# Kernel optimization log

Measured on AMD Instinct MI355X. Metric: run time of the kernel, lower is better.

## Reference

```python
import jax, jax.numpy as jnp
import numpy as np

N_RAYS = 65536
COUNT_CYCLE = (32, 64, 128, 256)  # ragged per-ray sample counts, avg 120
N_TOTAL = N_RAYS // len(COUNT_CYCLE) * sum(COUNT_CYCLE)  # 7,864,320


def _build_rays_a():
    counts = np.tile(np.array(COUNT_CYCLE, dtype=np.int32), N_RAYS // len(COUNT_CYCLE))
    starts = np.concatenate([[0], np.cumsum(counts)[:-1]]).astype(np.int32)
    ray_idx = np.arange(N_RAYS, dtype=np.int32)
    return jnp.asarray(np.stack([ray_idx, starts, counts], axis=1))


def setup_inputs() -> dict:
    key = jax.random.key(0)
    k1, k2, k3, k4 = jax.random.split(key, 4)
    sigmas = jax.random.uniform(k1, (N_TOTAL,), dtype=jnp.float32) * 2.0   # nonneg densities
    rgbs = jax.random.uniform(k2, (N_TOTAL, 3), dtype=jnp.float32)
    deltas = jax.random.uniform(k3, (N_TOTAL,), dtype=jnp.float32) * 0.05  # step sizes
    ts = jnp.sort(jax.random.uniform(k4, (N_TOTAL,), dtype=jnp.float32)) * 4.0
    rays_a = _build_rays_a()
    T_threshold = jnp.array([1e-4], dtype=jnp.float32)
    return {"sigmas": sigmas, "rgbs": rgbs, "deltas": deltas, "ts": ts,
            "rays_a": rays_a, "T_threshold": T_threshold}


def reference(sigmas, rgbs, deltas, ts, rays_a, T_threshold):
    """Per-ray alpha compositing with early termination (T >= thr).

    Within a ray, transmittance T is the exclusive product of (1 - a) with
    a = 1 - exp(-sigma*delta), i.e. T = exp(-cumsum_excl(sigma*delta)).
    Since T is monotone non-increasing, the kernel's sequential early-exit
    (skip samples once T < thr) equals masking with the prefix T >= thr.
    """
    n_rays = rays_a.shape[0]
    n = sigmas.shape[0]
    starts = rays_a[:, 1]
    # ray id of every flat sample (segments are contiguous, sorted starts)
    rid = jnp.searchsorted(starts, jnp.arange(n, dtype=starts.dtype), side="right") - 1

    sd = sigmas * deltas                      # [N]
    cs = jnp.cumsum(sd)
    excl = cs - sd                            # exclusive cumsum over the flat buffer
    seg_base = jnp.where(starts > 0, cs[jnp.maximum(starts - 1, 0)], 0.0)  # [n_rays]
    T = jnp.exp(-(excl - seg_base[rid]))      # exclusive transmittance within ray

    a = 1.0 - jnp.exp(-sd)
    alive = T >= T_threshold[0]               # prefix mask == early exit
    w = jnp.where(alive, a * T, 0.0)          # per-sample weights (ws)

    opacity = jax.ops.segment_sum(w, rid, num_segments=n_rays)
    depth = jax.ops.segment_sum(w * ts, rid, num_segments=n_rays)
    rgb = jax.ops.segment_sum(w[:, None] * rgbs, rid, num_segments=n_rays)
    total_samples = jax.ops.segment_sum(alive.astype(jnp.int32), rid, num_segments=n_rays)
    return total_samples, opacity, depth, rgb, w
```

## Files before the change

kernel.cpp:

```cpp
#include <hip/hip_runtime.h>


__global__ __launch_bounds__(256) void vr_fwd_kernel(
    const float* __restrict__ sigmas,
    const float* __restrict__ rgbs,
    const float* __restrict__ deltas,
    const float* __restrict__ ts,
    const int*   __restrict__ rays_a,
    const float* __restrict__ thr_p,
    float* __restrict__ out,
    int n_rays)
{
    const int wid  = (int)((blockIdx.x * (unsigned)blockDim.x + threadIdx.x) >> 6);
    const int lane = (int)(threadIdx.x & 63u);
    if (wid >= n_rays) return;

    const int   start = rays_a[wid * 3 + 1];
    const int   count = rays_a[wid * 3 + 2];
    const float thr   = thr_p[0];

    float* __restrict__ out_counts  = out;
    float* __restrict__ out_opacity = out + n_rays;
    float* __restrict__ out_depth   = out + 2 * n_rays;
    float* __restrict__ out_rgb     = out + 3 * n_rays;
    float* __restrict__ out_w       = out + 6 * n_rays;

    float carry = 0.0f;
    float acc_n = 0.0f, acc_op = 0.0f, acc_d = 0.0f;
    float acc_r = 0.0f, acc_g = 0.0f, acc_b = 0.0f;

    for (int base = 0; base < count; base += 64) {
        const int  i     = base + lane;
        const bool valid = (i < count);
        const int  gi    = start + i;

        float sd = 0.0f;
        if (valid) sd = sigmas[gi] * deltas[gi];

        float scan = sd;
        #pragma unroll
        for (int off = 1; off < 64; off <<= 1) {
            float up = __shfl_up(scan, off, 64);
            if (lane >= off) scan += up;
        }
        const float total = __shfl(scan, 63, 64);
        const float excl  = carry + (scan - sd);
        carry += total;

        if (valid) {
            const float T     = __expf(-excl);
            const float a     = 1.0f - __expf(-sd);
            const bool  alive = (T >= thr);
            const float w     = alive ? a * T : 0.0f;
            out_w[gi] = w;
            if (alive) {
                acc_n  += 1.0f;
                acc_op += w;
                acc_d  += w * ts[gi];
                acc_r  += w * rgbs[gi * 3 + 0];
                acc_g  += w * rgbs[gi * 3 + 1];
                acc_b  += w * rgbs[gi * 3 + 2];
            }
        }
    }

    #pragma unroll
    for (int off = 32; off > 0; off >>= 1) {
        acc_n  += __shfl_down(acc_n,  off, 64);
        acc_op += __shfl_down(acc_op, off, 64);
        acc_d  += __shfl_down(acc_d,  off, 64);
        acc_r  += __shfl_down(acc_r,  off, 64);
        acc_g  += __shfl_down(acc_g,  off, 64);
        acc_b  += __shfl_down(acc_b,  off, 64);
    }

    if (lane == 0) {
        out_counts[wid]      = acc_n;
        out_opacity[wid]     = acc_op;
        out_depth[wid]       = acc_d;
        out_rgb[wid * 3 + 0] = acc_r;
        out_rgb[wid * 3 + 1] = acc_g;
        out_rgb[wid * 3 + 2] = acc_b;
    }
}

extern "C" void kernel_launch(void* const* d_in, const int* in_sizes, int n_in,
                              void* d_out, int out_size, void* d_ws, size_t ws_size,
                              hipStream_t stream) {
    const float* sigmas = (const float*)d_in[0];
    const float* rgbs   = (const float*)d_in[1];
    const float* deltas = (const float*)d_in[2];
    const float* ts     = (const float*)d_in[3];
    const int*   rays_a = (const int*)d_in[4];
    const float* thr    = (const float*)d_in[5];

    const int n_rays = in_sizes[4] / 3;
    float* out = (float*)d_out;

    const int blocks = (n_rays + 3) / 4;
    vr_fwd_kernel<<<blocks, 256, 0, stream>>>(sigmas, rgbs, deltas, ts, rays_a,
                                              thr, out, n_rays);
}
```

Baseline: 44.94 us.

## Process four samples per lane with vectorized float4 loads and stores

Each lane now handles four consecutive samples, loading sigmas, deltas, ts and the interleaved rgb values as float4 when the ray start is 4-aligned, and writing weights as float4. A local 4-element prefix sum feeds a single wave scan per 256 samples, and transmittance within a lane is updated by multiplying by exp(-sd) instead of a separate exp per sample. This cuts shuffle-scan steps and memory instructions per sample. In exchange it adds a scalar fallback path, and the multiplicative T update may differ slightly numerically from the exp-of-sum form.

```diff
diff --git a/kernel.cpp b/kernel.cpp
--- a/kernel.cpp
+++ b/kernel.cpp
@@ -11,13 +11,14 @@
     float* __restrict__ out,
     int n_rays)
 {
-    const int wid  = (int)((blockIdx.x * (unsigned)blockDim.x + threadIdx.x) >> 6);
+    const int wid  = (int)((blockIdx.x * 256u + threadIdx.x) >> 6);
     const int lane = (int)(threadIdx.x & 63u);
     if (wid >= n_rays) return;
 
     const int   start = rays_a[wid * 3 + 1];
     const int   count = rays_a[wid * 3 + 2];
     const float thr   = thr_p[0];
+    const bool  al4   = ((start & 3) == 0);
 
     float* __restrict__ out_counts  = out;
     float* __restrict__ out_opacity = out + n_rays;
@@ -29,38 +30,81 @@
     float acc_n = 0.0f, acc_op = 0.0f, acc_d = 0.0f;
     float acc_r = 0.0f, acc_g = 0.0f, acc_b = 0.0f;
 
-    for (int base = 0; base < count; base += 64) {
-        const int  i     = base + lane;
-        const bool valid = (i < count);
-        const int  gi    = start + i;
+    for (int base = 0; base < count; base += 256) {
+        const int li  = base + lane * 4;
+        const int gi  = start + li;
+        const int rem = count - li;
 
-        float sd = 0.0f;
-        if (valid) sd = sigmas[gi] * deltas[gi];
+        float sd[4] = {0.f, 0.f, 0.f, 0.f};
+        float tv[4] = {0.f, 0.f, 0.f, 0.f};
+        float cr[4] = {0.f, 0.f, 0.f, 0.f};
+        float cg[4] = {0.f, 0.f, 0.f, 0.f};
+        float cb[4] = {0.f, 0.f, 0.f, 0.f};
 
-        float scan = sd;
+        if (al4 && rem >= 4) {
+            const float4 sg = *reinterpret_cast<const float4*>(sigmas + gi);
+            const float4 dl = *reinterpret_cast<const float4*>(deltas + gi);
+            const float4 t4 = *reinterpret_cast<const float4*>(ts + gi);
+            sd[0] = sg.x * dl.x; sd[1] = sg.y * dl.y;
+            sd[2] = sg.z * dl.z; sd[3] = sg.w * dl.w;
+            tv[0] = t4.x; tv[1] = t4.y; tv[2] = t4.z; tv[3] = t4.w;
+            const float4* rp = reinterpret_cast<const float4*>(rgbs + 3 * gi);
+            const float4 A = rp[0], B = rp[1], C = rp[2];
+            cr[0] = A.x; cg[0] = A.y; cb[0] = A.z;
+            cr[1] = A.w; cg[1] = B.x; cb[1] = B.y;
+            cr[2] = B.z; cg[2] = B.w; cb[2] = C.x;
+            cr[3] = C.y; cg[3] = C.z; cb[3] = C.w;
+        } else if (rem > 0) {
+            #pragma unroll
+            for (int k = 0; k < 4; ++k) {
+                if (k < rem) {
+                    sd[k] = sigmas[gi + k] * deltas[gi + k];
+                    tv[k] = ts[gi + k];
+                    cr[k] = rgbs[3 * (gi + k) + 0];
+                    cg[k] = rgbs[3 * (gi + k) + 1];
+                    cb[k] = rgbs[3 * (gi + k) + 2];
+                }
+            }
+        }
+
+        const float p1 = sd[0] + sd[1];
+        const float p2 = p1 + sd[2];
+        const float p3 = p2 + sd[3];
+
+        float sc = p3;
         #pragma unroll
         for (int off = 1; off < 64; off <<= 1) {
-            float up = __shfl_up(scan, off, 64);
-            if (lane >= off) scan += up;
+            const float up = __shfl_up(sc, off, 64);
+            if (lane >= off) sc += up;
         }
-        const float total = __shfl(scan, 63, 64);
-        const float excl  = carry + (scan - sd);
-        carry += total;
+        const float wave_total = __shfl(sc, 63, 64);
+        const float lex = carry + (sc - p3);
+        carry += wave_total;
 
-        if (valid) {
-            const float T     = __expf(-excl);
-            const float a     = 1.0f - __expf(-sd);
+        float T = __expf(-lex);
+        float wv[4];
+        #pragma unroll
+        for (int k = 0; k < 4; ++k) {
+            const float e     = __expf(-sd[k]);
             const bool  alive = (T >= thr);
-            const float w     = alive ? a * T : 0.0f;
-            out_w[gi] = w;
-            if (alive) {
-                acc_n  += 1.0f;
-                acc_op += w;
-                acc_d  += w * ts[gi];
-                acc_r  += w * rgbs[gi * 3 + 0];
-                acc_g  += w * rgbs[gi * 3 + 1];
-                acc_b  += w * rgbs[gi * 3 + 2];
-            }
+            const float w     = alive ? (1.0f - e) * T : 0.0f;
+            wv[k] = w;
+            if (alive && k < rem) acc_n += 1.0f;
+            acc_op += w;
+            acc_d  += w * tv[k];
+            acc_r  += w * cr[k];
+            acc_g  += w * cg[k];
+            acc_b  += w * cb[k];
+            T *= e;
+        }
+
+        if (al4 && rem >= 4) {
+            *reinterpret_cast<float4*>(out_w + gi) =
+                make_float4(wv[0], wv[1], wv[2], wv[3]);
+        } else if (rem > 0) {
+            #pragma unroll
+            for (int k = 0; k < 4; ++k)
+                if (k < rem) out_w[gi + k] = wv[k];
         }
     }
 
```

Result: faster. 43.97 us (-2.1%).
